# Kernel optimization log

Measured on AMD Instinct MI355X. Metric: run time of the kernel, lower is better.

The kernel has to match this reference:

```python
import jax, jax.numpy as jnp
import numpy as np

B, T, C, NH = 2, 2048, 1024, 16
HD = C // NH  # 64


def _ln(x, g, b, eps=1e-5):
    m = x.mean(-1, keepdims=True)
    v = ((x - m) ** 2).mean(-1, keepdims=True)
    return (x - m) / jnp.sqrt(v + eps) * g + b


def _ff(x, w1, b1, w2, b2):
    # Linear -> exact (erf) GELU -> Linear; dropout=0 (identity)
    return jax.nn.gelu(x @ w1 + b1, approximate=False) @ w2 + b2


def setup_inputs() -> dict:
    key = jax.random.key(0)
    ks = jax.random.split(key, 16)
    s = 0.02
    f32 = jnp.float32
    return {
        "x": jax.random.normal(ks[0], (B, T, C), f32),
        # SelfAttn qkv projection (torch Linear stored transposed: (in, out))
        "w_attn": jax.random.normal(ks[1], (C, 3 * C), f32) * s,
        "b_attn": jnp.zeros((3 * C,), f32),
        # SelfAttn's internal FeedForward
        "wa1": jax.random.normal(ks[2], (C, 4 * C), f32) * s,
        "ba1": jnp.zeros((4 * C,), f32),
        "wa2": jax.random.normal(ks[3], (4 * C, C), f32) * s,
        "ba2": jnp.zeros((C,), f32),
        # Block ln1
        "g1": jnp.ones((C,), f32),
        "be1": jnp.zeros((C,), f32),
        # Block FeedForward
        "wf1": jax.random.normal(ks[4], (C, 4 * C), f32) * s,
        "bf1": jnp.zeros((4 * C,), f32),
        "wf2": jax.random.normal(ks[5], (4 * C, C), f32) * s,
        "bf2": jnp.zeros((C,), f32),
        # Block ln2
        "g2": jnp.ones((C,), f32),
        "be2": jnp.zeros((C,), f32),
    }


def reference(x, w_attn, b_attn, wa1, ba1, wa2, ba2, g1, be1,
              wf1, bf1, wf2, bf2, g2, be2):
    Bx, Tx, Cx = x.shape
    qkv = x @ w_attn + b_attn  # (B, T, 3C)
    # NOTE: original splits as K, Q, V (in that order)
    K, Q, V = jnp.split(qkv, 3, axis=-1)

    def heads(t):  # (B, T, C) -> (B, NH, T, HD)
        return t.reshape(Bx, Tx, NH, HD).transpose(0, 2, 1, 3)

    Q, K, V = heads(Q), heads(K), heads(V)
    att = jnp.einsum('bhqd,bhkd->bhqk', Q, K) / np.float32(np.sqrt(HD))
    mask = jnp.tril(jnp.ones((Tx, Tx), bool))  # causal
    att = jnp.where(mask, att, -jnp.inf)
    att = jax.nn.softmax(att, axis=-1)
    y = jnp.einsum('bhqk,bhkd->bhqd', att, V)
    y = y.transpose(0, 2, 1, 3).reshape(Bx, Tx, Cx)
    # SelfAttn applies its own FeedForward (no output projection)
    y = _ff(y, wa1, ba1, wa2, ba2)
    # Block: post-sublayer LayerNorm, additive residuals
    x = x + _ln(y, g1, be1)
    x = x + _ln(_ff(x, wf1, bf1, wf2, bf2), g2, be2)
    return x
```

## Files before the change

### kernel.cpp

```cpp
#include <hip/hip_runtime.h>
#include <hip/hip_bf16.h>
#include <math.h>

#define Bz 2
#define Tz 2048
#define Cz 1024
#define NHz 16
#define HDz 64
#define Mz (Bz*Tz)

typedef unsigned short u16;
typedef __attribute__((ext_vector_type(8))) short bf16x8;
typedef __attribute__((ext_vector_type(4))) float f32x4;

__device__ __forceinline__ float bf2f(u16 u){
  union { unsigned int i; float f; } v; v.i = ((unsigned int)u) << 16; return v.f;
}
__device__ __forceinline__ u16 f2bf(float f){
  union { float f; unsigned int i; } v; v.f = f;
  return (u16)((v.i + 0x7fffu + ((v.i >> 16) & 1u)) >> 16);
}
__device__ __forceinline__ unsigned pack_bf_trunc(float a, float b){
  union { float f; unsigned u; } ua, ub; ua.f = a; ub.f = b;
  return (ua.u >> 16) | (ub.u & 0xffff0000u);
}
__device__ __forceinline__ float gelu_fast(float x){
  float x3 = x * x * x;
  float z2 = 1.5957691216057308f * (x + 0.044715f * x3);
  float e  = __expf(z2);
  float t  = 1.f - 2.f / (e + 1.f);
  return 0.5f * x * (1.f + t);
}

__device__ __forceinline__ void glds16(const void* g, void* l){
  __builtin_amdgcn_global_load_lds(
      (const __attribute__((address_space(1))) void*)g,
      (__attribute__((address_space(3))) void*)l, 16, 0, 0);
}

__global__ __launch_bounds__(256) void cast4_kernel(const float* __restrict__ in,
                                                    u16* __restrict__ out, int n4){
  int i = blockIdx.x * 256 + threadIdx.x;
  if (i < n4) {
    float4 v = ((const float4*)in)[i];
    u16 t[4] = { f2bf(v.x), f2bf(v.y), f2bf(v.z), f2bf(v.w) };
    *(uint2*)&out[(size_t)i * 4] = *(const uint2*)t;
  }
}

__global__ __launch_bounds__(256) void transpose5_kernel(
    const float* __restrict__ s0, const float* __restrict__ s1,
    const float* __restrict__ s2, const float* __restrict__ s3,
    const float* __restrict__ s4,
    u16* __restrict__ d0, u16* __restrict__ d1, u16* __restrict__ d2,
    u16* __restrict__ d3, u16* __restrict__ d4){
  __shared__ float tile[32][33];
  const int t = blockIdx.x;
  const float* src; u16* dst; int K, N, local;
  if (t < 3072)       { src = s0; dst = d0; K = 1024; N = 3072; local = t; }
  else if (t < 7168)  { src = s1; dst = d1; K = 1024; N = 4096; local = t - 3072; }
  else if (t < 11264) { src = s2; dst = d2; K = 4096; N = 1024; local = t - 7168; }
  else if (t < 15360) { src = s3; dst = d3; K = 1024; N = 4096; local = t - 11264; }
  else                { src = s4; dst = d4; K = 4096; N = 1024; local = t - 15360; }
  const int NT = N >> 5;
  const int kb = (local / NT) * 32, nb = (local % NT) * 32;
  const int tx = threadIdx.x & 31, ty = threadIdx.x >> 5;
  #pragma unroll
  for (int r = ty; r < 32; r += 8)
    tile[r][tx] = src[(size_t)(kb + r) * N + nb + tx];
  __syncthreads();
  #pragma unroll
  for (int r = ty; r < 32; r += 8)
    dst[(size_t)(nb + r) * K + kb + tx] = f2bf(tile[tx][r]);
}

template<int ACT>
__global__ __launch_bounds__(256) void gemm_kernel(const u16* __restrict__ A,
                                                   const u16* __restrict__ Bt,
                                                   const float* __restrict__ bias,
                                                   u16* __restrict__ ob0,
                                                   u16* __restrict__ ob1,
                                                   int N, int lda, int klen){
  __shared__ __align__(16) u16 As[2][128 * 32];
  __shared__ __align__(16) u16 Bs[2][128 * 32];
  const int tid  = threadIdx.x;
  const int wave = tid >> 6, lane = tid & 63;
  const int wm = (wave & 1) * 64, wn = (wave >> 1) * 64;
  const int m0 = blockIdx.x * 128, n0 = blockIdx.y * 128;
  const int kz = blockIdx.z;
  const int cc = lane & 15, quad = lane >> 4;
  const int lko = quad * 8;

  const u16* Ak  = A  + (size_t)kz * klen;
  const u16* Btk = Bt + (size_t)kz * klen;

  f32x4 acc[4][4] = {};

  const int nk = klen / 64;
  for (int ki = 0; ki < nk; ki++) {
    const int k0 = ki * 64;
    __syncthreads();
    #pragma unroll
    for (int it = 0; it < 4; it++) {
      int ci = tid + it * 256;
      int half = ci >> 9, rem = ci & 511;
      int row = rem >> 2, c4 = rem & 3;
      int gofs = k0 + half * 32 + c4 * 8;
      glds16(Ak  + (size_t)(m0 + row) * lda + gofs, &As[half][row * 32 + c4 * 8]);
      glds16(Btk + (size_t)(n0 + row) * lda + gofs, &Bs[half][row * 32 + c4 * 8]);
    }
    __syncthreads();

    #pragma unroll
    for (int s = 0; s < 2; s++) {
      bf16x8 af[4], bfr[4];
      #pragma unroll
      for (int i = 0; i < 4; i++)
        af[i]  = *(const bf16x8*)&As[s][(wm + i * 16 + cc) * 32 + lko];
      #pragma unroll
      for (int j = 0; j < 4; j++)
        bfr[j] = *(const bf16x8*)&Bs[s][(wn + j * 16 + cc) * 32 + lko];
      #pragma unroll
      for (int i = 0; i < 4; i++)
        #pragma unroll
        for (int j = 0; j < 4; j++)
          acc[i][j] = __builtin_amdgcn_mfma_f32_16x16x32_bf16(af[i], bfr[j], acc[i][j], 0, 0, 0);
    }
  }

  const float* bias_k = (kz == 0) ? bias : nullptr;
  u16* ob = (kz == 0) ? ob0 : ob1;
  const int rbase = quad * 4;
  #pragma unroll
  for (int i = 0; i < 4; i++) {
    #pragma unroll
    for (int j = 0; j < 4; j++) {
      int col = n0 + wn + j * 16 + cc;
      float bv = bias_k ? bias_k[col] : 0.f;
      #pragma unroll
      for (int r = 0; r < 4; r++) {
        int row = m0 + wm + i * 16 + rbase + r;
        float v = acc[i][j][r] + bv;
        if (ACT == 1) v = gelu_fast(v);
        ob[(size_t)row * N + col] = f2bf(v);
      }
    }
  }
}

__global__ __launch_bounds__(256) void vtrans_kernel(const u16* __restrict__ qkv,
                                                     u16* __restrict__ Vtb){
  __shared__ u16 Vl[64 * 72];
  const int tid = threadIdx.x;
  const int t0 = blockIdx.x * 64, h = blockIdx.y, b = blockIdx.z;
  const int bh = b * NHz + h;
  #pragma unroll
  for (int it = 0; it < 2; it++) {
    int c = tid + it * 256;
    int row = c >> 3, g = c & 7;
    *(uint4*)&Vl[row * 72 + g * 8] =
        *(const uint4*)(qkv + (size_t)(b * Tz + t0 + row) * (3 * Cz) + 2 * Cz + h * 64 + g * 8);
  }
  __syncthreads();
  #pragma unroll
  for (int it = 0; it < 2; it++) {
    int c = tid + it * 256;
    int d = c >> 3, tg = c & 7;
    u16 tmp[8];
    #pragma unroll
    for (int e = 0; e < 8; e++) tmp[e] = Vl[(tg * 8 + e) * 72 + d];
    *(uint4*)&Vtb[((size_t)bh * 64 + d) * Tz + t0 + tg * 8] = *(const uint4*)tmp;
  }
}

__global__ __launch_bounds__(256) void attn_kernel(const u16* __restrict__ qkv,
                                                   const u16* __restrict__ Vtb,
                                                   u16* __restrict__ y){
  __shared__ __align__(16) u16 KV[2][2][64 * 64];
  __shared__ __align__(16) u16 Ps[64 * 72];
  const int tid = threadIdx.x;
  const int lane = tid & 63, wave = tid >> 6;
  const int cc = lane & 15, quad = lane >> 4;
  const int h = blockIdx.y, b = blockIdx.z;
  const int bh = b * NHz + h;
  const size_t rowb = (size_t)b * Tz;
  const int wq0 = wave * 16;

  int foff[4][2];
  const int sw0 = (quad ^ (cc & 7)) * 8;
  const int sw1 = ((4 + quad) ^ (cc & 7)) * 8;
  #pragma unroll
  for (int t = 0; t < 4; ++t) {
    foff[t][0] = (t * 16 + cc) * 64 + sw0;
    foff[t][1] = (t * 16 + cc) * 64 + sw1;
  }
  const int pswb = (wq0 + cc) * 72 + quad * 4;
  const int psr0 = (wq0 + cc) * 72 + quad * 8;
  const int psr1 = (wq0 + cc) * 72 + 32 + quad * 8;

  auto stage = [&](int i, int bsel) {
    const int k0s = i * 64;
    #pragma unroll
    for (int it = 0; it < 2; ++it) {
      int ci = tid + it * 256;
      int row = ci >> 3, g = ci & 7;
      int gs = g ^ (row & 7);
      glds16(qkv + (rowb + k0s + row) * (3 * Cz) + h * 64 + gs * 8, &KV[bsel][0][ci * 8]);
      glds16(Vtb + ((size_t)bh * 64 + row) * Tz + k0s + gs * 8,     &KV[bsel][1][ci * 8]);
    }
  };

  for (int ph = 0; ph < 2; ++ph) {
    const int qt = ph ? (31 - (int)blockIdx.x) : (int)blockIdx.x;
    const int q0t = qt * 64 + wq0;
    const int nkt = qt + 1;
    const int wqmax = q0t + 15;

    bf16x8 qf[2];
    #pragma unroll
    for (int s = 0; s < 2; ++s)
      qf[s] = *(const bf16x8*)(qkv + (rowb + q0t + cc) * (3 * Cz)
                               + Cz + h * 64 + s * 32 + quad * 8);
    f32x4 acc[4] = {};
    float lp = 0.f;

    if (ph) __syncthreads();
    stage(0, 0);

    for (int i = 0; i < nkt; ++i) {
      __syncthreads();
      if (i + 1 < nkt) stage(i + 1, (i + 1) & 1);
      const int sel = i & 1;
      const u16* Kl = KV[sel][0];
      const u16* Vl = KV[sel][1];
      const int k0 = i * 64;
      if (k0 > wqmax) continue;

      bf16x8 kf[4][2];
      #pragma unroll
      for (int kt = 0; kt < 4; ++kt) {
        kf[kt][0] = *(const bf16x8*)&Kl[foff[kt][0]];
        kf[kt][1] = *(const bf16x8*)&Kl[foff[kt][1]];
      }
      const int qbase = q0t;
      #pragma unroll
      for (int kt = 0; kt < 4; ++kt) {
        const int kbase = k0 + kt * 16;
        uint2 pk;
        if (kbase > qbase + 15) {
          pk.x = 0u; pk.y = 0u;
        } else {
          f32x4 st = __builtin_amdgcn_mfma_f32_16x16x32_bf16(
              kf[kt][0], qf[0], (f32x4){0.f, 0.f, 0.f, 0.f}, 0, 0, 0);
          st = __builtin_amdgcn_mfma_f32_16x16x32_bf16(kf[kt][1], qf[1], st, 0, 0, 0);
          if (kbase + 15 > qbase) {
            const int kq = kbase + quad * 4, ql = qbase + cc;
            st[0] = (kq     <= ql) ? st[0] : -1e30f;
            st[1] = (kq + 1 <= ql) ? st[1] : -1e30f;
            st[2] = (kq + 2 <= ql) ? st[2] : -1e30f;
            st[3] = (kq + 3 <= ql) ? st[3] : -1e30f;
          }
          float p0 = __expf(fmaf(st[0], 0.125f, -16.f));
          float p1 = __expf(fmaf(st[1], 0.125f, -16.f));
          float p2 = __expf(fmaf(st[2], 0.125f, -16.f));
          float p3 = __expf(fmaf(st[3], 0.125f, -16.f));
          lp += (p0 + p1) + (p2 + p3);
          pk.x = pack_bf_trunc(p0, p1);
          pk.y = pack_bf_trunc(p2, p3);
        }
        *(uint2*)&Ps[pswb + kt * 16] = pk;
      }
      bf16x8 pf0 = *(const bf16x8*)&Ps[psr0];
      bf16x8 pf1 = *(const bf16x8*)&Ps[psr1];
      #pragma unroll
      for (int jd = 0; jd < 4; ++jd) {
        bf16x8 vf0 = *(const bf16x8*)&Vl[foff[jd][0]];
        bf16x8 vf1 = *(const bf16x8*)&Vl[foff[jd][1]];
        acc[jd] = __builtin_amdgcn_mfma_f32_16x16x32_bf16(pf0, vf0, acc[jd], 0, 0, 0);
        acc[jd] = __builtin_amdgcn_mfma_f32_16x16x32_bf16(pf1, vf1, acc[jd], 0, 0, 0);
      }
    }

    lp += __shfl_xor(lp, 16, 64);
    lp += __shfl_xor(lp, 32, 64);
    float inv[4];
    #pragma unroll
    for (int r = 0; r < 4; ++r) inv[r] = 1.f / __shfl(lp, quad * 4 + r, 64);
    #pragma unroll
    for (int jd = 0; jd < 4; ++jd)
      #pragma unroll
      for (int r = 0; r < 4; ++r) {
        int qrow = q0t + quad * 4 + r;
        y[(rowb + qrow) * Cz + h * 64 + jd * 16 + cc] = f2bf(acc[jd][r] * inv[r]);
      }
  }
}

__global__ __launch_bounds__(256) void ln_resid_kernel(const float* __restrict__ xf,
                                                       const u16* __restrict__ xb16,
                                                       const u16* __restrict__ y1,
                                                       const u16* __restrict__ y2,
                                                       const float* __restrict__ g,
                                                       const float* __restrict__ be,
                                                       float* __restrict__ outf,
                                                       u16* __restrict__ outb){
  const int row = blockIdx.x;
  const int c0 = threadIdx.x * 4;
  const size_t base = (size_t)row * Cz + c0;
  uint2 p1 = *(const uint2*)(y1 + base);
  float4 v;
  v.x = bf2f((u16)(p1.x & 0xffff)); v.y = bf2f((u16)(p1.x >> 16));
  v.z = bf2f((u16)(p1.y & 0xffff)); v.w = bf2f((u16)(p1.y >> 16));
  if (y2) {
    uint2 p2 = *(const uint2*)(y2 + base);
    v.x += bf2f((u16)(p2.x & 0xffff)); v.y += bf2f((u16)(p2.x >> 16));
    v.z += bf2f((u16)(p2.y & 0xffff)); v.w += bf2f((u16)(p2.y >> 16));
  }
  float s  = v.x + v.y + v.z + v.w;
  float s2 = v.x*v.x + v.y*v.y + v.z*v.z + v.w*v.w;
  #pragma unroll
  for (int off = 32; off > 0; off >>= 1) {
    s  += __shfl_down(s,  off);
    s2 += __shfl_down(s2, off);
  }
  __shared__ float ps[4], ps2[4];
  int wave = threadIdx.x >> 6, lane = threadIdx.x & 63;
  if (lane == 0) { ps[wave] = s; ps2[wave] = s2; }
  __syncthreads();
  s  = ps[0]  + ps[1]  + ps[2]  + ps[3];
  s2 = ps2[0] + ps2[1] + ps2[2] + ps2[3];
  const float mean = s * (1.f / Cz);
  const float var  = s2 * (1.f / Cz) - mean * mean;
  const float rstd = rsqrtf(var + 1e-5f);
  float4 xv;
  if (xf) {
    xv = *(const float4*)(xf + base);
  } else {
    uint2 px = *(const uint2*)(xb16 + base);
    xv.x = bf2f((u16)(px.x & 0xffff)); xv.y = bf2f((u16)(px.x >> 16));
    xv.z = bf2f((u16)(px.y & 0xffff)); xv.w = bf2f((u16)(px.y >> 16));
  }
  float4 gv = *(const float4*)(g + c0);
  float4 bv = *(const float4*)(be + c0);
  float4 ov;
  ov.x = xv.x + (v.x - mean) * rstd * gv.x + bv.x;
  ov.y = xv.y + (v.y - mean) * rstd * gv.y + bv.y;
  ov.z = xv.z + (v.z - mean) * rstd * gv.z + bv.z;
  ov.w = xv.w + (v.w - mean) * rstd * gv.w + bv.w;
  if (outf) *(float4*)(outf + base) = ov;
  if (outb) {
    u16 t[4] = { f2bf(ov.x), f2bf(ov.y), f2bf(ov.z), f2bf(ov.w) };
    *(ulonglong1*)&outb[base] = *(const ulonglong1*)t;
  }
}

extern "C" void kernel_launch(void* const* d_in, const int* in_sizes, int n_in,
                              void* d_out, int out_size, void* d_ws, size_t ws_size,
                              hipStream_t stream) {
  const float* x      = (const float*)d_in[0];
  const float* w_attn = (const float*)d_in[1];
  const float* b_attn = (const float*)d_in[2];
  const float* wa1    = (const float*)d_in[3];
  const float* ba1    = (const float*)d_in[4];
  const float* wa2    = (const float*)d_in[5];
  const float* ba2    = (const float*)d_in[6];
  const float* g1     = (const float*)d_in[7];
  const float* be1    = (const float*)d_in[8];
  const float* wf1    = (const float*)d_in[9];
  const float* bf1    = (const float*)d_in[10];
  const float* wf2    = (const float*)d_in[11];
  const float* bf2    = (const float*)d_in[12];
  const float* g2     = (const float*)d_in[13];
  const float* be2    = (const float*)d_in[14];
  float* out = (float*)d_out;

  char* ws = (char*)d_ws;
  size_t off = 0;
  auto alloc = [&](size_t bytes) { size_t o = off; off += (bytes + 255) & ~(size_t)255; return o; };
  u16* qkvb    = (u16*)(ws + alloc((size_t)Mz * 3 * Cz * 2));
  u16* ybuf    = (u16*)(ws + alloc((size_t)Mz * Cz * 2));
  u16* xb      = (u16*)(ws + alloc((size_t)Mz * Cz * 2));
  u16* wT_attn = (u16*)(ws + alloc((size_t)3 * Cz * Cz * 2));
  u16* wT_a1   = (u16*)(ws + alloc((size_t)4 * Cz * Cz * 2));
  u16* Vtb     = (u16*)(ws + alloc((size_t)Bz * NHz * HDz * Tz * 2));
  u16* wT_a2   = (u16*)(ws + alloc((size_t)4 * Cz * Cz * 2));
  u16* wT_f1   = (u16*)(ws + alloc((size_t)4 * Cz * Cz * 2));
  u16* wT_f2   = (u16*)(ws + alloc((size_t)4 * Cz * Cz * 2));
  u16* hbuf    = (u16*)(ws + alloc((size_t)Mz * 4 * Cz * 2));
  u16* pb0     = (u16*)(ws + alloc((size_t)Mz * Cz * 2));
  u16* pb1     = (u16*)(ws + alloc((size_t)Mz * Cz * 2));
  u16* x1b     = (u16*)(ws + alloc((size_t)Mz * Cz * 2));
  alloc(256);
  (void)ws_size; (void)in_sizes; (void)n_in; (void)out_size;

  cast4_kernel<<<(Mz * Cz / 4 + 255) / 256, 256, 0, stream>>>(x, xb, Mz * Cz / 4);
  transpose5_kernel<<<19456, 256, 0, stream>>>(w_attn, wa1, wa2, wf1, wf2,
                                               wT_attn, wT_a1, wT_a2, wT_f1, wT_f2);

  gemm_kernel<0><<<dim3(Mz/128, 3*Cz/128, 1), 256, 0, stream>>>(xb, wT_attn, b_attn,
      qkvb, nullptr, 3*Cz, Cz, Cz);

  vtrans_kernel<<<dim3(Tz/64, NHz, Bz), 256, 0, stream>>>(qkvb, Vtb);
  attn_kernel<<<dim3(16, NHz, Bz), 256, 0, stream>>>(qkvb, Vtb, ybuf);

  gemm_kernel<1><<<dim3(Mz/128, 4*Cz/128, 1), 256, 0, stream>>>(ybuf, wT_a1, ba1,
      hbuf, nullptr, 4*Cz, Cz, Cz);
  gemm_kernel<0><<<dim3(Mz/128, Cz/128, 2), 256, 0, stream>>>(hbuf, wT_a2, ba2,
      pb0, pb1, Cz, 4*Cz, 2*Cz);

  ln_resid_kernel<<<Mz, 256, 0, stream>>>(x, nullptr, pb0, pb1, g1, be1,
                                          nullptr, x1b);

  gemm_kernel<1><<<dim3(Mz/128, 4*Cz/128, 1), 256, 0, stream>>>(x1b, wT_f1, bf1,
      hbuf, nullptr, 4*Cz, Cz, Cz);
  gemm_kernel<0><<<dim3(Mz/128, Cz/128, 2), 256, 0, stream>>>(hbuf, wT_f2, bf2,
      pb0, pb1, Cz, 4*Cz, 2*Cz);

  ln_resid_kernel<<<Mz, 256, 0, stream>>>(nullptr, x1b, pb0, pb1, g2, be2,
                                          out, nullptr);
}
```

Baseline: 480.9 us.

## Replace 128x128 GEMM with pipelined 256x256 tile kernel and 4-way split-K

Replaces the 128x128 bf16 MFMA GEMM with a 512-thread 256x256-tile kernel. The new kernel uses swizzled LDS layout, double-buffered global-to-LDS loads interleaved with MFMA quadrants under explicit barriers and vmcnt waits, setprio around MFMA bursts, and a grid remap for cache locality. The down-projection GEMMs now split K four ways into a contiguous partial buffer, and the LayerNorm kernel sums the four partials. The larger tiles cut global and LDS traffic per FLOP, at the cost of fewer workgroups, higher register and LDS pressure, and extra partial-sum memory traffic.

```diff
diff --git a/kernel.cpp b/kernel.cpp
--- a/kernel.cpp
+++ b/kernel.cpp
@@ -37,6 +37,13 @@
       (const __attribute__((address_space(1))) void*)g,
       (__attribute__((address_space(3))) void*)l, 16, 0, 0);
 }
+
+__device__ __forceinline__ void pbar(){
+  asm volatile("" ::: "memory");
+  __builtin_amdgcn_s_barrier();
+  asm volatile("" ::: "memory");
+}
+#define VMCNT(n) asm volatile("s_waitcnt vmcnt(" #n ")" ::: "memory")
 
 __global__ __launch_bounds__(256) void cast4_kernel(const float* __restrict__ in,
                                                     u16* __restrict__ out, int n4){
@@ -75,77 +82,139 @@
 }
 
 template<int ACT>
-__global__ __launch_bounds__(256) void gemm_kernel(const u16* __restrict__ A,
-                                                   const u16* __restrict__ Bt,
-                                                   const float* __restrict__ bias,
-                                                   u16* __restrict__ ob0,
-                                                   u16* __restrict__ ob1,
-                                                   int N, int lda, int klen){
-  __shared__ __align__(16) u16 As[2][128 * 32];
-  __shared__ __align__(16) u16 Bs[2][128 * 32];
+__global__ __launch_bounds__(512, 2) void gemm256_kernel(const u16* __restrict__ A,
+                                                         const u16* __restrict__ Bt,
+                                                         const float* __restrict__ bias,
+                                                         u16* __restrict__ ob,
+                                                         int N, int lda, int klen){
+  __shared__ __align__(16) u16 As[2][256 * 64];
+  __shared__ __align__(16) u16 Bs[2][256 * 64];
   const int tid  = threadIdx.x;
-  const int wave = tid >> 6, lane = tid & 63;
-  const int wm = (wave & 1) * 64, wn = (wave >> 1) * 64;
-  const int m0 = blockIdx.x * 128, n0 = blockIdx.y * 128;
-  const int kz = blockIdx.z;
+  const int lane = tid & 63;
+  const int wave = tid >> 6;
   const int cc = lane & 15, quad = lane >> 4;
-  const int lko = quad * 8;
-
-  const u16* Ak  = A  + (size_t)kz * klen;
-  const u16* Btk = Bt + (size_t)kz * klen;
-
-  f32x4 acc[4][4] = {};
-
-  const int nk = klen / 64;
-  for (int ki = 0; ki < nk; ki++) {
-    const int k0 = ki * 64;
-    __syncthreads();
-    #pragma unroll
-    for (int it = 0; it < 4; it++) {
-      int ci = tid + it * 256;
-      int half = ci >> 9, rem = ci & 511;
-      int row = rem >> 2, c4 = rem & 3;
-      int gofs = k0 + half * 32 + c4 * 8;
-      glds16(Ak  + (size_t)(m0 + row) * lda + gofs, &As[half][row * 32 + c4 * 8]);
-      glds16(Btk + (size_t)(n0 + row) * lda + gofs, &Bs[half][row * 32 + c4 * 8]);
-    }
-    __syncthreads();
-
-    #pragma unroll
-    for (int s = 0; s < 2; s++) {
-      bf16x8 af[4], bfr[4];
-      #pragma unroll
-      for (int i = 0; i < 4; i++)
-        af[i]  = *(const bf16x8*)&As[s][(wm + i * 16 + cc) * 32 + lko];
-      #pragma unroll
-      for (int j = 0; j < 4; j++)
-        bfr[j] = *(const bf16x8*)&Bs[s][(wn + j * 16 + cc) * 32 + lko];
-      #pragma unroll
-      for (int i = 0; i < 4; i++)
+  const int wm = (wave >> 2) * 128;
+  const int wn = (wave & 3) * 64;
+
+  int flat = blockIdx.x + gridDim.x * blockIdx.y;
+  const int nwg = gridDim.x * gridDim.y;
+  flat = (flat & 7) * (nwg >> 3) + (flat >> 3);
+  const int m0 = (flat & 15) * 256;
+  const int n0 = (flat >> 4) * 256;
+
+  const u16* Ak  = A  + (size_t)blockIdx.z * klen;
+  const u16* Btk = Bt + (size_t)blockIdx.z * klen;
+
+  int srow[2], scol[2];
+  #pragma unroll
+  for (int rnd = 0; rnd < 2; ++rnd) {
+    const int ci = tid + rnd * 512;
+    const int r = ci >> 3, cg = ci & 7;
+    srow[rnd] = r;
+    scol[rnd] = (cg ^ (r & 7)) * 8;
+  }
+  int colsw[2];
+  #pragma unroll
+  for (int s = 0; s < 2; ++s)
+    colsw[s] = (s * 32 + quad * 8) ^ ((cc & 7) << 3);
+
+  const auto stA = [&](int h, int t) {
+    u16* dst = &As[t & 1][h * 8192];
+    const u16* src = Ak + (size_t)(m0 + h * 128) * lda + t * 64;
+    #pragma unroll
+    for (int rnd = 0; rnd < 2; ++rnd)
+      glds16(src + (size_t)srow[rnd] * lda + scol[rnd], dst + (tid + rnd * 512) * 8);
+  };
+  const auto stB = [&](int h, int t) {
+    u16* dst = &Bs[t & 1][h * 8192];
+    const u16* src = Btk + (size_t)(n0 + h * 128) * lda + t * 64;
+    #pragma unroll
+    for (int rnd = 0; rnd < 2; ++rnd)
+      glds16(src + (size_t)srow[rnd] * lda + scol[rnd], dst + (tid + rnd * 512) * 8);
+  };
+
+  bf16x8 af[4][2];
+  bf16x8 bfr[2][2][2];
+  f32x4 acc[2][2][4][2] = {};
+
+  const auto rdA = [&](int qa, int bsel) {
+    #pragma unroll
+    for (int f = 0; f < 4; ++f)
+      #pragma unroll
+      for (int s = 0; s < 2; ++s)
+        af[f][s] = *(const bf16x8*)&As[bsel][(wm + qa * 64 + f * 16 + cc) * 64 + colsw[s]];
+  };
+  const auto rdB = [&](int qb, int bsel) {
+    #pragma unroll
+    for (int f = 0; f < 2; ++f)
+      #pragma unroll
+      for (int s = 0; s < 2; ++s)
+        bfr[qb][f][s] = *(const bf16x8*)&Bs[bsel][(wn + qb * 32 + f * 16 + cc) * 64 + colsw[s]];
+  };
+  const auto mf16 = [&](int qa, int qb) {
+    __builtin_amdgcn_s_setprio(1);
+    #pragma unroll
+    for (int s = 0; s < 2; ++s)
+      #pragma unroll
+      for (int am = 0; am < 4; ++am)
         #pragma unroll
-        for (int j = 0; j < 4; j++)
-          acc[i][j] = __builtin_amdgcn_mfma_f32_16x16x32_bf16(af[i], bfr[j], acc[i][j], 0, 0, 0);
-    }
-  }
-
-  const float* bias_k = (kz == 0) ? bias : nullptr;
-  u16* ob = (kz == 0) ? ob0 : ob1;
-  const int rbase = quad * 4;
-  #pragma unroll
-  for (int i = 0; i < 4; i++) {
-    #pragma unroll
-    for (int j = 0; j < 4; j++) {
-      int col = n0 + wn + j * 16 + cc;
-      float bv = bias_k ? bias_k[col] : 0.f;
-      #pragma unroll
-      for (int r = 0; r < 4; r++) {
-        int row = m0 + wm + i * 16 + rbase + r;
-        float v = acc[i][j][r] + bv;
-        if (ACT == 1) v = gelu_fast(v);
-        ob[(size_t)row * N + col] = f2bf(v);
+        for (int bn = 0; bn < 2; ++bn)
+          acc[qa][qb][am][bn] = __builtin_amdgcn_mfma_f32_16x16x32_bf16(
+              af[am][s], bfr[qb][bn][s], acc[qa][qb][am][bn], 0, 0, 0);
+    __builtin_amdgcn_s_setprio(0);
+  };
+
+  stA(0, 0); stB(0, 0); stA(1, 0); stB(1, 0);
+  stA(0, 1); stB(1, 1);
+  VMCNT(4);
+  pbar();
+
+  const int nIter = klen >> 7;
+  for (int i = 0; i < nIter; ++i) {
+    const int t = 2 * i;
+    const bool more = (i + 1 < nIter);
+    rdA(0, 0); rdB(0, 0); stA(1, t + 1);
+    pbar(); mf16(0, 0); pbar();
+    rdB(1, 0); stB(0, t + 1);
+    pbar(); mf16(0, 1); pbar();
+    rdA(1, 0); if (more) stA(0, t + 2);
+    pbar(); mf16(1, 1); pbar();
+    if (more) stB(1, t + 2);
+    pbar(); mf16(1, 0);
+    if (more) { VMCNT(4); } else { VMCNT(0); }
+    pbar();
+    rdA(0, 1); rdB(0, 1); if (more) stA(1, t + 2);
+    pbar(); mf16(0, 0); pbar();
+    rdB(1, 1); if (more) stB(0, t + 2);
+    pbar(); mf16(0, 1); pbar();
+    rdA(1, 1); if (more) stA(0, t + 3);
+    pbar(); mf16(1, 1); pbar();
+    if (more) stB(1, t + 3);
+    pbar(); mf16(1, 0);
+    if (more) { VMCNT(4); }
+    pbar();
+  }
+
+  u16* obz = ob + (size_t)blockIdx.z * ((size_t)Mz * N);
+  const float* bp = (blockIdx.z == 0) ? bias : nullptr;
+  #pragma unroll
+  for (int qa = 0; qa < 2; ++qa)
+    #pragma unroll
+    for (int qb = 0; qb < 2; ++qb)
+      #pragma unroll
+      for (int bn = 0; bn < 2; ++bn) {
+        const int col = n0 + wn + qb * 32 + bn * 16 + cc;
+        const float bv = bp ? bp[col] : 0.f;
+        #pragma unroll
+        for (int am = 0; am < 4; ++am)
+          #pragma unroll
+          for (int r = 0; r < 4; ++r) {
+            const int row = m0 + wm + qa * 64 + am * 16 + quad * 4 + r;
+            float v = acc[qa][qb][am][bn][r] + bv;
+            if (ACT == 1) v = gelu_fast(v);
+            obz[(size_t)row * N + col] = f2bf(v);
+          }
       }
-    }
-  }
 }
 
 __global__ __launch_bounds__(256) void vtrans_kernel(const u16* __restrict__ qkv,
@@ -298,8 +367,7 @@
 
 __global__ __launch_bounds__(256) void ln_resid_kernel(const float* __restrict__ xf,
                                                        const u16* __restrict__ xb16,
-                                                       const u16* __restrict__ y1,
-                                                       const u16* __restrict__ y2,
+                                                       const u16* __restrict__ yp,
                                                        const float* __restrict__ g,
                                                        const float* __restrict__ be,
                                                        float* __restrict__ outf,
@@ -307,14 +375,12 @@
   const int row = blockIdx.x;
   const int c0 = threadIdx.x * 4;
   const size_t base = (size_t)row * Cz + c0;
-  uint2 p1 = *(const uint2*)(y1 + base);
-  float4 v;
-  v.x = bf2f((u16)(p1.x & 0xffff)); v.y = bf2f((u16)(p1.x >> 16));
-  v.z = bf2f((u16)(p1.y & 0xffff)); v.w = bf2f((u16)(p1.y >> 16));
-  if (y2) {
-    uint2 p2 = *(const uint2*)(y2 + base);
-    v.x += bf2f((u16)(p2.x & 0xffff)); v.y += bf2f((u16)(p2.x >> 16));
-    v.z += bf2f((u16)(p2.y & 0xffff)); v.w += bf2f((u16)(p2.y >> 16));
+  float4 v; v.x = 0.f; v.y = 0.f; v.z = 0.f; v.w = 0.f;
+  #pragma unroll
+  for (int p = 0; p < 4; ++p) {
+    uint2 pp = *(const uint2*)(yp + (size_t)p * ((size_t)Mz * Cz) + base);
+    v.x += bf2f((u16)(pp.x & 0xffff)); v.y += bf2f((u16)(pp.x >> 16));
+    v.z += bf2f((u16)(pp.y & 0xffff)); v.w += bf2f((u16)(pp.y >> 16));
   }
   float s  = v.x + v.y + v.z + v.w;
   float s2 = v.x*v.x + v.y*v.y + v.z*v.z + v.w*v.w;
@@ -387,8 +453,7 @@
   u16* wT_f1   = (u16*)(ws + alloc((size_t)4 * Cz * Cz * 2));
   u16* wT_f2   = (u16*)(ws + alloc((size_t)4 * Cz * Cz * 2));
   u16* hbuf    = (u16*)(ws + alloc((size_t)Mz * 4 * Cz * 2));
-  u16* pb0     = (u16*)(ws + alloc((size_t)Mz * Cz * 2));
-  u16* pb1     = (u16*)(ws + alloc((size_t)Mz * Cz * 2));
+  u16* pb      = (u16*)(ws + alloc((size_t)4 * Mz * Cz * 2));
   u16* x1b     = (u16*)(ws + alloc((size_t)Mz * Cz * 2));
   alloc(256);
   (void)ws_size; (void)in_sizes; (void)n_in; (void)out_size;
@@ -397,25 +462,25 @@
   transpose5_kernel<<<19456, 256, 0, stream>>>(w_attn, wa1, wa2, wf1, wf2,
                                                wT_attn, wT_a1, wT_a2, wT_f1, wT_f2);
 
-  gemm_kernel<0><<<dim3(Mz/128, 3*Cz/128, 1), 256, 0, stream>>>(xb, wT_attn, b_attn,
-      qkvb, nullptr, 3*Cz, Cz, Cz);
+  gemm256_kernel<0><<<dim3(16, 12, 1), 512, 0, stream>>>(xb, wT_attn, b_attn,
+      qkvb, 3*Cz, Cz, Cz);
 
   vtrans_kernel<<<dim3(Tz/64, NHz, Bz), 256, 0, stream>>>(qkvb, Vtb);
   attn_kernel<<<dim3(16, NHz, Bz), 256, 0, stream>>>(qkvb, Vtb, ybuf);
 
-  gemm_kernel<1><<<dim3(Mz/128, 4*Cz/128, 1), 256, 0, stream>>>(ybuf, wT_a1, ba1,
-      hbuf, nullptr, 4*Cz, Cz, Cz);
-  gemm_kernel<0><<<dim3(Mz/128, Cz/128, 2), 256, 0, stream>>>(hbuf, wT_a2, ba2,
-      pb0, pb1, Cz, 4*Cz, 2*Cz);
-
-  ln_resid_kernel<<<Mz, 256, 0, stream>>>(x, nullptr, pb0, pb1, g1, be1,
+  gemm256_kernel<1><<<dim3(16, 16, 1), 512, 0, stream>>>(ybuf, wT_a1, ba1,
+      hbuf, 4*Cz, Cz, Cz);
+  gemm256_kernel<0><<<dim3(16, 4, 4), 512, 0, stream>>>(hbuf, wT_a2, ba2,
+      pb, Cz, 4*Cz, Cz);
+
+  ln_resid_kernel<<<Mz, 256, 0, stream>>>(x, nullptr, pb, g1, be1,
                                           nullptr, x1b);
 
-  gemm_kernel<1><<<dim3(Mz/128, 4*Cz/128, 1), 256, 0, stream>>>(x1b, wT_f1, bf1,
-      hbuf, nullptr, 4*Cz, Cz, Cz);
-  gemm_kernel<0><<<dim3(Mz/128, Cz/128, 2), 256, 0, stream>>>(hbuf, wT_f2, bf2,
-      pb0, pb1, Cz, 4*Cz, 2*Cz);
-
-  ln_resid_kernel<<<Mz, 256, 0, stream>>>(nullptr, x1b, pb0, pb1, g2, be2,
+  gemm256_kernel<1><<<dim3(16, 16, 1), 512, 0, stream>>>(x1b, wT_f1, bf1,
+      hbuf, 4*Cz, Cz, Cz);
+  gemm256_kernel<0><<<dim3(16, 4, 4), 512, 0, stream>>>(hbuf, wT_f2, bf2,
+      pb, Cz, 4*Cz, Cz);
+
+  ln_resid_kernel<<<Mz, 256, 0, stream>>>(nullptr, x1b, pb, g2, be2,
                                           out, nullptr);
 }
```

Result: faster. 462.8 us (-3.8%).
